# Performance work log

Hardware: AMD Instinct MI355X
Metric: run time of the kernel (lower is better)

Reference implementation:

```python
import jax, jax.numpy as jnp
import numpy as np

T, B, D, H = 1024, 256, 64, 128  # seq_len, batch, x_dim, dim_RNN (= dense dims)


def _linear_params(key, fan_in, fan_out):
    # torch nn.Linear/nn.RNN default init: U(-1/sqrt(fan_in), 1/sqrt(fan_in))
    s = 1.0 / np.sqrt(fan_in)
    kw, kb = jax.random.split(key)
    W = jax.random.uniform(kw, (fan_out, fan_in), minval=-s, maxval=s, dtype=jnp.float32)
    b = jax.random.uniform(kb, (fan_out,), minval=-s, maxval=s, dtype=jnp.float32)
    return W, b


def setup_inputs() -> dict:
    key = jax.random.key(0)
    kx, k1, k2, k3, k4, k5 = jax.random.split(key, 6)
    x = jax.random.normal(kx, (T, B, D), dtype=jnp.float32)
    W_x, b_x = _linear_params(k1, D, H)      # feature_extractor_x: Linear(D->H)
    W_ih, b_ih = _linear_params(k2, H, H)    # RNN input-hidden
    W_hh, b_hh = _linear_params(k3, H, H)    # RNN hidden-hidden
    W_h, b_h = _linear_params(k4, H, H)      # mlp_h_x: Linear(H->H)
    W_g, b_g = _linear_params(k5, H, D)      # gen_out: Linear(H->D)
    return {"x": x, "W_x": W_x, "b_x": b_x, "W_ih": W_ih, "b_ih": b_ih,
            "W_hh": W_hh, "b_hh": b_hh, "W_h": W_h, "b_h": b_h,
            "W_g": W_g, "b_g": b_g}


def reference(x, W_x, b_x, W_ih, b_ih, W_hh, b_hh, W_h, b_h, W_g, b_g):
    # feature extractor applied to all timesteps at once (as in the original)
    feat = jnp.tanh(x @ W_x.T + b_x)                       # [T, B, H]
    batch = x.shape[1]
    h0 = jnp.zeros((batch, W_hh.shape[0]), dtype=x.dtype)  # [B, H]

    def step(h, f_t):
        # y_t is produced from h BEFORE the recurrence update (y[0] uses h=0)
        y_t = jnp.tanh(h @ W_h.T + b_h) @ W_g.T + b_g      # [B, D]
        h_next = jnp.tanh(f_t @ W_ih.T + b_ih + h @ W_hh.T + b_hh)
        return h_next, y_t

    _, y = jax.lax.scan(step, h0, feat)                    # y: [T, B, D]
    return y
```

## Files before the change

### kernel.cpp

```cpp
#include <hip/hip_runtime.h>


#define T_SEQ 1024
#define B_SZ  256
#define D_IN  64
#define H_DIM 128

typedef __attribute__((ext_vector_type(8))) _Float16 half8;
typedef __attribute__((ext_vector_type(4))) _Float16 half4;
typedef __attribute__((ext_vector_type(4))) float f32x4;

__device__ __forceinline__ float fast_tanh(float x) {
  float ax = __builtin_fabsf(x);
  float e  = __builtin_amdgcn_exp2f(ax * -2.8853900817779268f);
  float r  = (1.0f - e) * __builtin_amdgcn_rcpf(1.0f + e);
  return __builtin_copysignf(r, x);
}

__device__ __forceinline__ void barrier_lds_only() {
  __asm__ __volatile__("" ::: "memory");
  __builtin_amdgcn_s_waitcnt(0xC07F);
  __builtin_amdgcn_s_barrier();
  __asm__ __volatile__("" ::: "memory");
}

__device__ __forceinline__ half8 pack_h8(float4 a, float4 b) {
  half8 s = { (_Float16)a.x, (_Float16)a.y, (_Float16)a.z, (_Float16)a.w,
              (_Float16)b.x, (_Float16)b.y, (_Float16)b.z, (_Float16)b.w };
  return s;
}
__device__ __forceinline__ half4 cvt_h4(float4 a) {
  half4 s = { (_Float16)a.x, (_Float16)a.y, (_Float16)a.z, (_Float16)a.w };
  return s;
}
__device__ __forceinline__ void split_h8(float4 a, float4 b, half8& hi, half8& lo) {
  hi = pack_h8(a, b);
  float4 ra = { a.x - (float)hi[0], a.y - (float)hi[1],
                a.z - (float)hi[2], a.w - (float)hi[3] };
  float4 rb = { b.x - (float)hi[4], b.y - (float)hi[5],
                b.z - (float)hi[6], b.w - (float)hi[7] };
  lo = pack_h8(ra, rb);
}

__device__ __forceinline__ float add_xor1(float x) {
  int v = __builtin_amdgcn_mov_dpp(__float_as_int(x), 0xB1, 0xF, 0xF, true);
  return x + __int_as_float(v);
}
__device__ __forceinline__ float add_xor2(float x) {
  int v = __builtin_amdgcn_mov_dpp(__float_as_int(x), 0x4E, 0xF, 0xF, true);
  return x + __int_as_float(v);
}
__device__ __forceinline__ float add_mirror8(float x) {
  int v = __builtin_amdgcn_mov_dpp(__float_as_int(x), 0x141, 0xF, 0xF, true);
  return x + __int_as_float(v);
}
__device__ __forceinline__ float dot4(float4 w, float4 h) {
  return fmaf(w.x, h.x, fmaf(w.y, h.y, fmaf(w.z, h.z, w.w * h.w)));
}

__global__ __launch_bounds__(512) void k_fused(
    const float* __restrict__ x,   const float* __restrict__ Wx,
    const float* __restrict__ bx,  const float* __restrict__ Wih,
    const float* __restrict__ bih, const float* __restrict__ Whh,
    const float* __restrict__ bhh, const float* __restrict__ Wh,
    const float* __restrict__ bh,  const float* __restrict__ Wg,
    const float* __restrict__ bg,  float* __restrict__ y)
{
  __shared__ __align__(16) float    hbuf[2][192];
  __shared__ __align__(16) float    zringT[4][H_DIM][20];
  __shared__ __align__(16) _Float16 hring[4][16][136];
  __shared__ __align__(16) _Float16 xt_h[16][72];
  __shared__ __align__(16) _Float16 xt_l[16][72];
  __shared__ __align__(16) _Float16 fm_h[16][136];
  __shared__ __align__(16) _Float16 fm_l[16][136];
  __shared__ __align__(16) _Float16 tpm[16][136];

  const int tid = threadIdx.x;
  const int b   = blockIdx.x;
  const int wv  = tid >> 6;

  if (wv < 4) {
    const int jg = tid >> 3, ks = tid & 7, k0p = ks * 24;
    const bool writer = (ks < 4);
    const int j_out = jg + (ks & 3) * 32;
    const int j_pad = j_out + ((j_out >> 4) << 3);

    float4 w[4][4];
#pragma unroll
    for (int r = 0; r < 4; ++r) {
      const float4* wg = (const float4*)(Whh + (jg + r*32)*H_DIM + ks*16);
#pragma unroll
      for (int m = 0; m < 4; ++m) w[r][m] = wg[m];
    }
    if (tid < 128) hbuf[0][tid + ((tid >> 4) << 3)] = 0.f;
    else           hring[0][0][tid - 128] = (_Float16)0.f;

    __builtin_amdgcn_s_setprio(1);
    for (int i = 0; i < 5; ++i) barrier_lds_only();

    for (int g = 0; g < 64; ++g) {
      float zbuf[16];
      if (writer) {
        const float* zp = &zringT[g & 3][j_out][0];
        const float4 z0 = *(const float4*)(zp + 0);
        const float4 z1 = *(const float4*)(zp + 4);
        const float4 z2 = *(const float4*)(zp + 8);
        const float4 z3 = *(const float4*)(zp + 12);
        zbuf[0]=z0.x;  zbuf[1]=z0.y;  zbuf[2]=z0.z;  zbuf[3]=z0.w;
        zbuf[4]=z1.x;  zbuf[5]=z1.y;  zbuf[6]=z1.z;  zbuf[7]=z1.w;
        zbuf[8]=z2.x;  zbuf[9]=z2.y;  zbuf[10]=z2.z; zbuf[11]=z2.w;
        zbuf[12]=z3.x; zbuf[13]=z3.y; zbuf[14]=z3.z; zbuf[15]=z3.w;
      }
#pragma unroll
      for (int s = 0; s < 16; ++s) {
        const float* h = hbuf[s & 1];
        float4 h0 = *(const float4*)&h[k0p];
        float4 h1 = *(const float4*)&h[k0p + 4];
        float4 h2 = *(const float4*)&h[k0p + 8];
        float4 h3 = *(const float4*)&h[k0p + 12];

        float a[4];
#pragma unroll
        for (int r = 0; r < 4; ++r) {
          float p0 = dot4(w[r][0], h0);
          float p1 = dot4(w[r][1], h1);
          float p2 = dot4(w[r][2], h2);
          float p3 = dot4(w[r][3], h3);
          a[r] = (p0 + p1) + (p2 + p3);
        }
#pragma unroll
        for (int r = 0; r < 4; ++r) {
          a[r] = add_xor1(a[r]);
          a[r] = add_xor2(a[r]);
          a[r] = add_mirror8(a[r]);
        }
        if (writer) {
          float v  = a[ks] + zbuf[s];
          float hn = fast_tanh(v);
          hbuf[(s & 1) ^ 1][j_pad] = hn;
          const int tn = g*16 + s + 1;
          hring[(tn >> 4) & 3][tn & 15][j_out] = (_Float16)hn;
        }
        barrier_lds_only();
      }
    }
    barrier_lds_only();

  } else if (wv < 6) {
    const int l = tid & 63, ln = l & 15, kg = l >> 4;
    const int pw = wv - 4;
    const int xr0 = pw*8 + kg;

    half8 wxh[4][2], wxl[4][2];
    float bxr[4], b2r[4];
#pragma unroll
    for (int nt = 0; nt < 4; ++nt) {
      const int ro = (pw*4 + nt)*16 + ln;
#pragma unroll
      for (int kf = 0; kf < 2; ++kf) {
        const float* wp = Wx + ro*D_IN + kf*32 + kg*8;
        split_h8(*(const float4*)wp, *(const float4*)(wp + 4),
                 wxh[nt][kf], wxl[nt][kf]);
      }
      bxr[nt] = bx[ro];
      b2r[nt] = bih[ro] + bhh[ro];
    }

    float4 xa0, xa1;
    float4 lw[16];

    auto loadx = [&](int t0) {
      xa0 = *(const float4*)(x + ((long)(t0 + xr0    )*B_SZ + b)*D_IN + ln*4);
      xa1 = *(const float4*)(x + ((long)(t0 + xr0 + 4)*B_SZ + b)*D_IN + ln*4);
    };
    auto cvtx = [&]() {
      half4 h0 = cvt_h4(xa0);
      float4 r0 = { xa0.x - (float)h0[0], xa0.y - (float)h0[1],
                    xa0.z - (float)h0[2], xa0.w - (float)h0[3] };
      *(half4*)&xt_h[xr0][ln*4] = h0;
      *(half4*)&xt_l[xr0][ln*4] = cvt_h4(r0);
      half4 h1 = cvt_h4(xa1);
      float4 r1 = { xa1.x - (float)h1[0], xa1.y - (float)h1[1],
                    xa1.z - (float)h1[2], xa1.w - (float)h1[3] };
      *(half4*)&xt_h[xr0 + 4][ln*4] = h1;
      *(half4*)&xt_l[xr0 + 4][ln*4] = cvt_h4(r1);
    };
    auto st1 = [&]() {
      half8 a1h[2], a1l[2];
#pragma unroll
      for (int kf = 0; kf < 2; ++kf) {
        a1h[kf] = *(const half8*)&xt_h[ln][kf*32 + kg*8];
        a1l[kf] = *(const half8*)&xt_l[ln][kf*32 + kg*8];
      }
#pragma unroll
      for (int nt = 0; nt < 4; ++nt) {
        f32x4 acc = {0.f, 0.f, 0.f, 0.f};
#pragma unroll
        for (int kf = 0; kf < 2; ++kf) {
          acc = __builtin_amdgcn_mfma_f32_16x16x32_f16(a1h[kf], wxh[nt][kf], acc, 0, 0, 0);
          acc = __builtin_amdgcn_mfma_f32_16x16x32_f16(a1l[kf], wxh[nt][kf], acc, 0, 0, 0);
          acc = __builtin_amdgcn_mfma_f32_16x16x32_f16(a1h[kf], wxl[nt][kf], acc, 0, 0, 0);
        }
#pragma unroll
        for (int c = 0; c < 4; ++c) {
          float v = fast_tanh(acc[c] + bxr[nt]);
          _Float16 vh = (_Float16)v;
          fm_h[kg*4 + c][(pw*4 + nt)*16 + ln] = vh;
          fm_l[kg*4 + c][(pw*4 + nt)*16 + ln] = (_Float16)(v - (float)vh);
        }
      }
    };
    auto ld2 = [&](int nt0) {
#pragma unroll
      for (int i = 0; i < 2; ++i) {
        const int ro = (pw*4 + nt0 + i)*16 + ln;
#pragma unroll
        for (int kf = 0; kf < 4; ++kf) {
          const float* wp = Wih + ro*H_DIM + kf*32 + kg*8;
          lw[i*8 + kf*2 + 0] = *(const float4*)wp;
          lw[i*8 + kf*2 + 1] = *(const float4*)(wp + 4);
        }
      }
    };
    auto use2 = [&](int nt0, int slot) {
      half8 a2h[4], a2l[4];
#pragma unroll
      for (int kf = 0; kf < 4; ++kf) {
        a2h[kf] = *(const half8*)&fm_h[ln][kf*32 + kg*8];
        a2l[kf] = *(const half8*)&fm_l[ln][kf*32 + kg*8];
      }
#pragma unroll
      for (int i = 0; i < 2; ++i) {
        const int nt = nt0 + i;
        const int ro = (pw*4 + nt)*16 + ln;
        f32x4 acc = { b2r[nt], b2r[nt], b2r[nt], b2r[nt] };
#pragma unroll
        for (int kf = 0; kf < 4; ++kf) {
          half8 bh_, bl_;
          split_h8(lw[i*8 + kf*2], lw[i*8 + kf*2 + 1], bh_, bl_);
          acc = __builtin_amdgcn_mfma_f32_16x16x32_f16(a2h[kf], bh_, acc, 0, 0, 0);
          acc = __builtin_amdgcn_mfma_f32_16x16x32_f16(a2l[kf], bh_, acc, 0, 0, 0);
          acc = __builtin_amdgcn_mfma_f32_16x16x32_f16(a2h[kf], bl_, acc, 0, 0, 0);
        }
        *(f32x4*)&zringT[slot][ro][kg*4] = acc;
      }
    };

    loadx(0);
    cvtx(); loadx(16);            barrier_lds_only();
    st1();                        barrier_lds_only();
    ld2(0); use2(0, 0); ld2(2); use2(2, 0);
    cvtx(); loadx(32);            barrier_lds_only();
    st1();                        barrier_lds_only();
    ld2(0); use2(0, 1); ld2(2); use2(2, 1);
                                  barrier_lds_only();

    for (int g = 0; g < 64; ++g) {
      const bool act = (g <= 61);
      const int slot = (g + 2) & 3;
      if (act) cvtx();
      if (g <= 60) loadx((g + 3) * 16);
      barrier_lds_only();
      if (act) { ld2(0); st1(); }
      barrier_lds_only();
      if (act) { use2(0, slot); ld2(2); }
      barrier_lds_only();
      if (act) use2(2, slot);
      barrier_lds_only();
      for (int s = 4; s < 16; ++s) barrier_lds_only();
    }
    barrier_lds_only();

  } else {
    const int l = tid & 63, ln = l & 15, kg = l >> 4;
    const int cw = wv - 6;

    float bhr[4], bgr[2];
#pragma unroll
    for (int nt = 0; nt < 4; ++nt) bhr[nt] = bh[(cw*4 + nt)*16 + ln];
#pragma unroll
    for (int n2 = 0; n2 < 2; ++n2) bgr[n2] = bg[(cw*2 + n2)*16 + ln];

    float4 lwc[16];

    auto ldc1 = [&](int nt0) {
#pragma unroll
      for (int i = 0; i < 2; ++i) {
        const int ro = (cw*4 + nt0 + i)*16 + ln;
#pragma unroll
        for (int kf = 0; kf < 4; ++kf) {
          const float* wp = Wh + ro*H_DIM + kf*32 + kg*8;
          lwc[i*8 + kf*2 + 0] = *(const float4*)wp;
          lwc[i*8 + kf*2 + 1] = *(const float4*)(wp + 4);
        }
      }
    };
    auto usec1 = [&](int nt0, int slot) {
      half8 ah[4];
#pragma unroll
      for (int kf = 0; kf < 4; ++kf)
        ah[kf] = *(const half8*)&hring[slot][ln][kf*32 + kg*8];
#pragma unroll
      for (int i = 0; i < 2; ++i) {
        const int nt = nt0 + i;
        f32x4 acc = {0.f, 0.f, 0.f, 0.f};
#pragma unroll
        for (int kf = 0; kf < 4; ++kf) {
          half8 bh_, bl_;
          split_h8(lwc[i*8 + kf*2], lwc[i*8 + kf*2 + 1], bh_, bl_);
          acc = __builtin_amdgcn_mfma_f32_16x16x32_f16(ah[kf], bh_, acc, 0, 0, 0);
          acc = __builtin_amdgcn_mfma_f32_16x16x32_f16(ah[kf], bl_, acc, 0, 0, 0);
        }
#pragma unroll
        for (int c = 0; c < 4; ++c)
          tpm[kg*4 + c][(cw*4 + nt)*16 + ln] =
              (_Float16)fast_tanh(acc[c] + bhr[nt]);
      }
    };
    auto ldc2 = [&]() {
#pragma unroll
      for (int i = 0; i < 2; ++i) {
        const int ro = (cw*2 + i)*16 + ln;
#pragma unroll
        for (int kf = 0; kf < 4; ++kf) {
          const float* wp = Wg + ro*H_DIM + kf*32 + kg*8;
          lwc[i*8 + kf*2 + 0] = *(const float4*)wp;
          lwc[i*8 + kf*2 + 1] = *(const float4*)(wp + 4);
        }
      }
    };
    auto usec2 = [&](int t0) {
      half8 atp[4];
#pragma unroll
      for (int kf = 0; kf < 4; ++kf)
        atp[kf] = *(const half8*)&tpm[ln][kf*32 + kg*8];
#pragma unroll
      for (int n2 = 0; n2 < 2; ++n2) {
        f32x4 acc = { bgr[n2], bgr[n2], bgr[n2], bgr[n2] };
#pragma unroll
        for (int kf = 0; kf < 4; ++kf) {
          half8 bh_, bl_;
          split_h8(lwc[n2*8 + kf*2], lwc[n2*8 + kf*2 + 1], bh_, bl_);
          acc = __builtin_amdgcn_mfma_f32_16x16x32_f16(atp[kf], bh_, acc, 0, 0, 0);
          acc = __builtin_amdgcn_mfma_f32_16x16x32_f16(atp[kf], bl_, acc, 0, 0, 0);
        }
#pragma unroll
        for (int c = 0; c < 4; ++c)
          y[((long)(t0 + kg*4 + c)*B_SZ + b)*D_IN + (cw*2 + n2)*16 + ln] = acc[c];
      }
    };

    for (int i = 0; i < 5; ++i) barrier_lds_only();

    for (int g = 0; g < 64; ++g) {
      const bool act = (g >= 1);
      const int slot = (g - 1) & 3;
      const int t0 = (g - 1) * 16;
      barrier_lds_only();
      barrier_lds_only();
      barrier_lds_only();
      barrier_lds_only();
      barrier_lds_only();
      barrier_lds_only();
      if (act) ldc1(0);
      barrier_lds_only();
      if (act) { usec1(0, slot); ldc1(2); }
      barrier_lds_only();
      if (act) { usec1(2, slot); ldc2(); }
      barrier_lds_only();
      barrier_lds_only();
      if (act) usec2(t0);
      barrier_lds_only();
      for (int s = 11; s < 16; ++s) barrier_lds_only();
    }
    ldc1(0); usec1(0, 3); ldc1(2); usec1(2, 3);
    barrier_lds_only();
    ldc2(); usec2(63 * 16);
  }
}

extern "C" void kernel_launch(void* const* d_in, const int* in_sizes, int n_in,
                              void* d_out, int out_size, void* d_ws, size_t ws_size,
                              hipStream_t stream) {
  const float* x   = (const float*)d_in[0];
  const float* Wx  = (const float*)d_in[1];
  const float* bx  = (const float*)d_in[2];
  const float* Wih = (const float*)d_in[3];
  const float* bih = (const float*)d_in[4];
  const float* Whh = (const float*)d_in[5];
  const float* bhh = (const float*)d_in[6];
  const float* Wh  = (const float*)d_in[7];
  const float* bh  = (const float*)d_in[8];
  const float* Wg  = (const float*)d_in[9];
  const float* bg  = (const float*)d_in[10];
  float* y = (float*)d_out;

  k_fused<<<B_SZ, 512, 0, stream>>>(x, Wx, bx, Wih, bih, Whh, bhh,
                                    Wh, bh, Wg, bg, y);
}
```

Baseline: 655.5 us.

## Split producer and consumer warp work into finer per-tile stages across barriers

```diff
diff --git a/kernel.cpp b/kernel.cpp
--- a/kernel.cpp
+++ b/kernel.cpp
@@ -167,7 +167,8 @@
     }
 
     float4 xa0, xa1;
-    float4 lw[16];
+    half8 a1h[2], a1l[2], a2h[4], a2l[4];
+    float4 lwA[8], lwB[8];
 
     auto loadx = [&](int t0) {
       xa0 = *(const float4*)(x + ((long)(t0 + xr0    )*B_SZ + b)*D_IN + ln*4);
@@ -185,15 +186,16 @@
       *(half4*)&xt_h[xr0 + 4][ln*4] = h1;
       *(half4*)&xt_l[xr0 + 4][ln*4] = cvt_h4(r1);
     };
-    auto st1 = [&]() {
-      half8 a1h[2], a1l[2];
+    auto rd_a1 = [&]() {
 #pragma unroll
       for (int kf = 0; kf < 2; ++kf) {
         a1h[kf] = *(const half8*)&xt_h[ln][kf*32 + kg*8];
         a1l[kf] = *(const half8*)&xt_l[ln][kf*32 + kg*8];
       }
-#pragma unroll
-      for (int nt = 0; nt < 4; ++nt) {
+    };
+    auto st1_h = [&](int nt0) {
+#pragma unroll
+      for (int nt = nt0; nt < nt0 + 2; ++nt) {
         f32x4 acc = {0.f, 0.f, 0.f, 0.f};
 #pragma unroll
         for (int kf = 0; kf < 2; ++kf) {
@@ -210,64 +212,72 @@
         }
       }
     };
-    auto ld2 = [&](int nt0) {
-#pragma unroll
-      for (int i = 0; i < 2; ++i) {
-        const int ro = (pw*4 + nt0 + i)*16 + ln;
-#pragma unroll
-        for (int kf = 0; kf < 4; ++kf) {
-          const float* wp = Wih + ro*H_DIM + kf*32 + kg*8;
-          lw[i*8 + kf*2 + 0] = *(const float4*)wp;
-          lw[i*8 + kf*2 + 1] = *(const float4*)(wp + 4);
-        }
-      }
-    };
-    auto use2 = [&](int nt0, int slot) {
-      half8 a2h[4], a2l[4];
+    auto rd_a2 = [&]() {
 #pragma unroll
       for (int kf = 0; kf < 4; ++kf) {
         a2h[kf] = *(const half8*)&fm_h[ln][kf*32 + kg*8];
         a2l[kf] = *(const half8*)&fm_l[ln][kf*32 + kg*8];
       }
-#pragma unroll
-      for (int i = 0; i < 2; ++i) {
-        const int nt = nt0 + i;
-        const int ro = (pw*4 + nt)*16 + ln;
-        f32x4 acc = { b2r[nt], b2r[nt], b2r[nt], b2r[nt] };
-#pragma unroll
-        for (int kf = 0; kf < 4; ++kf) {
-          half8 bh_, bl_;
-          split_h8(lw[i*8 + kf*2], lw[i*8 + kf*2 + 1], bh_, bl_);
-          acc = __builtin_amdgcn_mfma_f32_16x16x32_f16(a2h[kf], bh_, acc, 0, 0, 0);
-          acc = __builtin_amdgcn_mfma_f32_16x16x32_f16(a2l[kf], bh_, acc, 0, 0, 0);
-          acc = __builtin_amdgcn_mfma_f32_16x16x32_f16(a2h[kf], bl_, acc, 0, 0, 0);
-        }
-        *(f32x4*)&zringT[slot][ro][kg*4] = acc;
-      }
+    };
+    auto ldq = [&](float4* lw, int nt) {
+      const int ro = (pw*4 + nt)*16 + ln;
+      const float* wp0 = Wih + ro*H_DIM;
+#pragma unroll
+      for (int kf = 0; kf < 4; ++kf) {
+        lw[kf*2 + 0] = *(const float4*)(wp0 + kf*32 + kg*8);
+        lw[kf*2 + 1] = *(const float4*)(wp0 + kf*32 + kg*8 + 4);
+      }
+    };
+    auto use2_q = [&](const float4* lw, int nt, int slot) {
+      const int ro = (pw*4 + nt)*16 + ln;
+      f32x4 acc = { b2r[nt], b2r[nt], b2r[nt], b2r[nt] };
+#pragma unroll
+      for (int kf = 0; kf < 4; ++kf) {
+        half8 bh_, bl_;
+        split_h8(lw[kf*2], lw[kf*2 + 1], bh_, bl_);
+        acc = __builtin_amdgcn_mfma_f32_16x16x32_f16(a2h[kf], bh_, acc, 0, 0, 0);
+        acc = __builtin_amdgcn_mfma_f32_16x16x32_f16(a2l[kf], bh_, acc, 0, 0, 0);
+        acc = __builtin_amdgcn_mfma_f32_16x16x32_f16(a2h[kf], bl_, acc, 0, 0, 0);
+      }
+      *(f32x4*)&zringT[slot][ro][kg*4] = acc;
     };
 
     loadx(0);
-    cvtx(); loadx(16);            barrier_lds_only();
-    st1();                        barrier_lds_only();
-    ld2(0); use2(0, 0); ld2(2); use2(2, 0);
-    cvtx(); loadx(32);            barrier_lds_only();
-    st1();                        barrier_lds_only();
-    ld2(0); use2(0, 1); ld2(2); use2(2, 1);
-                                  barrier_lds_only();
+    cvtx(); loadx(16);                       barrier_lds_only();
+    rd_a1(); st1_h(0); st1_h(2);             barrier_lds_only();
+    rd_a2();
+    ldq(lwA, 0); use2_q(lwA, 0, 0);
+    ldq(lwA, 1); use2_q(lwA, 1, 0);
+    ldq(lwA, 2); use2_q(lwA, 2, 0);
+    ldq(lwA, 3); use2_q(lwA, 3, 0);
+    cvtx(); loadx(32);                       barrier_lds_only();
+    rd_a1(); st1_h(0); st1_h(2);             barrier_lds_only();
+    rd_a2();
+    ldq(lwA, 0); use2_q(lwA, 0, 1);
+    ldq(lwA, 1); use2_q(lwA, 1, 1);
+    ldq(lwA, 2); use2_q(lwA, 2, 1);
+    ldq(lwA, 3); use2_q(lwA, 3, 1);
+                                             barrier_lds_only();
 
     for (int g = 0; g < 64; ++g) {
       const bool act = (g <= 61);
       const int slot = (g + 2) & 3;
-      if (act) cvtx();
+      if (act) { cvtx(); ldq(lwA, 0); }
       if (g <= 60) loadx((g + 3) * 16);
       barrier_lds_only();
-      if (act) { ld2(0); st1(); }
-      barrier_lds_only();
-      if (act) { use2(0, slot); ld2(2); }
-      barrier_lds_only();
-      if (act) use2(2, slot);
-      barrier_lds_only();
-      for (int s = 4; s < 16; ++s) barrier_lds_only();
+      if (act) { rd_a1(); st1_h(0); ldq(lwB, 1); }
+      barrier_lds_only();
+      if (act) st1_h(2);
+      barrier_lds_only();
+      if (act) { rd_a2(); use2_q(lwA, 0, slot); ldq(lwA, 2); }
+      barrier_lds_only();
+      if (act) { use2_q(lwB, 1, slot); ldq(lwB, 3); }
+      barrier_lds_only();
+      if (act) use2_q(lwA, 2, slot);
+      barrier_lds_only();
+      if (act) use2_q(lwB, 3, slot);
+      barrier_lds_only();
+      for (int s = 7; s < 16; ++s) barrier_lds_only();
     }
     barrier_lds_only();
 
@@ -281,73 +291,65 @@
 #pragma unroll
     for (int n2 = 0; n2 < 2; ++n2) bgr[n2] = bg[(cw*2 + n2)*16 + ln];
 
-    float4 lwc[16];
-
-    auto ldc1 = [&](int nt0) {
-#pragma unroll
-      for (int i = 0; i < 2; ++i) {
-        const int ro = (cw*4 + nt0 + i)*16 + ln;
-#pragma unroll
-        for (int kf = 0; kf < 4; ++kf) {
-          const float* wp = Wh + ro*H_DIM + kf*32 + kg*8;
-          lwc[i*8 + kf*2 + 0] = *(const float4*)wp;
-          lwc[i*8 + kf*2 + 1] = *(const float4*)(wp + 4);
-        }
-      }
-    };
-    auto usec1 = [&](int nt0, int slot) {
-      half8 ah[4];
+    half8 ah[4], atp[4];
+    float4 lcA[8], lcB[8];
+
+    auto rd_ah = [&](int slot) {
 #pragma unroll
       for (int kf = 0; kf < 4; ++kf)
         ah[kf] = *(const half8*)&hring[slot][ln][kf*32 + kg*8];
-#pragma unroll
-      for (int i = 0; i < 2; ++i) {
-        const int nt = nt0 + i;
-        f32x4 acc = {0.f, 0.f, 0.f, 0.f};
-#pragma unroll
-        for (int kf = 0; kf < 4; ++kf) {
-          half8 bh_, bl_;
-          split_h8(lwc[i*8 + kf*2], lwc[i*8 + kf*2 + 1], bh_, bl_);
-          acc = __builtin_amdgcn_mfma_f32_16x16x32_f16(ah[kf], bh_, acc, 0, 0, 0);
-          acc = __builtin_amdgcn_mfma_f32_16x16x32_f16(ah[kf], bl_, acc, 0, 0, 0);
-        }
-#pragma unroll
-        for (int c = 0; c < 4; ++c)
-          tpm[kg*4 + c][(cw*4 + nt)*16 + ln] =
-              (_Float16)fast_tanh(acc[c] + bhr[nt]);
-      }
-    };
-    auto ldc2 = [&]() {
-#pragma unroll
-      for (int i = 0; i < 2; ++i) {
-        const int ro = (cw*2 + i)*16 + ln;
-#pragma unroll
-        for (int kf = 0; kf < 4; ++kf) {
-          const float* wp = Wg + ro*H_DIM + kf*32 + kg*8;
-          lwc[i*8 + kf*2 + 0] = *(const float4*)wp;
-          lwc[i*8 + kf*2 + 1] = *(const float4*)(wp + 4);
-        }
-      }
-    };
-    auto usec2 = [&](int t0) {
-      half8 atp[4];
+    };
+    auto ldc = [&](float4* lc, int nt) {
+      const int ro = (cw*4 + nt)*16 + ln;
+      const float* wp0 = Wh + ro*H_DIM;
+#pragma unroll
+      for (int kf = 0; kf < 4; ++kf) {
+        lc[kf*2 + 0] = *(const float4*)(wp0 + kf*32 + kg*8);
+        lc[kf*2 + 1] = *(const float4*)(wp0 + kf*32 + kg*8 + 4);
+      }
+    };
+    auto usec1_q = [&](const float4* lc, int nt) {
+      f32x4 acc = {0.f, 0.f, 0.f, 0.f};
+#pragma unroll
+      for (int kf = 0; kf < 4; ++kf) {
+        half8 bh_, bl_;
+        split_h8(lc[kf*2], lc[kf*2 + 1], bh_, bl_);
+        acc = __builtin_amdgcn_mfma_f32_16x16x32_f16(ah[kf], bh_, acc, 0, 0, 0);
+        acc = __builtin_amdgcn_mfma_f32_16x16x32_f16(ah[kf], bl_, acc, 0, 0, 0);
+      }
+#pragma unroll
+      for (int c = 0; c < 4; ++c)
+        tpm[kg*4 + c][(cw*4 + nt)*16 + ln] =
+            (_Float16)fast_tanh(acc[c] + bhr[nt]);
+    };
+    auto ldcg = [&]() {
+#pragma unroll
+      for (int kf = 0; kf < 4; ++kf) {
+        const float* wp0 = Wg + ((cw*2 + 0)*16 + ln)*H_DIM + kf*32 + kg*8;
+        lcA[kf*2 + 0] = *(const float4*)wp0;
+        lcA[kf*2 + 1] = *(const float4*)(wp0 + 4);
+        const float* wp1 = Wg + ((cw*2 + 1)*16 + ln)*H_DIM + kf*32 + kg*8;
+        lcB[kf*2 + 0] = *(const float4*)wp1;
+        lcB[kf*2 + 1] = *(const float4*)(wp1 + 4);
+      }
+    };
+    auto rd_atp = [&]() {
 #pragma unroll
       for (int kf = 0; kf < 4; ++kf)
         atp[kf] = *(const half8*)&tpm[ln][kf*32 + kg*8];
-#pragma unroll
-      for (int n2 = 0; n2 < 2; ++n2) {
-        f32x4 acc = { bgr[n2], bgr[n2], bgr[n2], bgr[n2] };
-#pragma unroll
-        for (int kf = 0; kf < 4; ++kf) {
-          half8 bh_, bl_;
-          split_h8(lwc[n2*8 + kf*2], lwc[n2*8 + kf*2 + 1], bh_, bl_);
-          acc = __builtin_amdgcn_mfma_f32_16x16x32_f16(atp[kf], bh_, acc, 0, 0, 0);
-          acc = __builtin_amdgcn_mfma_f32_16x16x32_f16(atp[kf], bl_, acc, 0, 0, 0);
-        }
-#pragma unroll
-        for (int c = 0; c < 4; ++c)
-          y[((long)(t0 + kg*4 + c)*B_SZ + b)*D_IN + (cw*2 + n2)*16 + ln] = acc[c];
-      }
+    };
+    auto usec2_h = [&](const float4* lc, int n2, int t0) {
+      f32x4 acc = { bgr[n2], bgr[n2], bgr[n2], bgr[n2] };
+#pragma unroll
+      for (int kf = 0; kf < 4; ++kf) {
+        half8 bh_, bl_;
+        split_h8(lc[kf*2], lc[kf*2 + 1], bh_, bl_);
+        acc = __builtin_amdgcn_mfma_f32_16x16x32_f16(atp[kf], bh_, acc, 0, 0, 0);
+        acc = __builtin_amdgcn_mfma_f32_16x16x32_f16(atp[kf], bl_, acc, 0, 0, 0);
+      }
+#pragma unroll
+      for (int c = 0; c < 4; ++c)
+        y[((long)(t0 + kg*4 + c)*B_SZ + b)*D_IN + (cw*2 + n2)*16 + ln] = acc[c];
     };
 
     for (int i = 0; i < 5; ++i) barrier_lds_only();
@@ -362,20 +364,32 @@
       barrier_lds_only();
       barrier_lds_only();
       barrier_lds_only();
-      if (act) ldc1(0);
-      barrier_lds_only();
-      if (act) { usec1(0, slot); ldc1(2); }
-      barrier_lds_only();
-      if (act) { usec1(2, slot); ldc2(); }
-      barrier_lds_only();
-      barrier_lds_only();
-      if (act) usec2(t0);
-      barrier_lds_only();
-      for (int s = 11; s < 16; ++s) barrier_lds_only();
+      if (act) { rd_ah(slot); ldc(lcA, 0); }
+      barrier_lds_only();
+      if (act) { usec1_q(lcA, 0); ldc(lcB, 1); }
+      barrier_lds_only();
+      if (act) { usec1_q(lcB, 1); ldc(lcA, 2); }
+      barrier_lds_only();
+      if (act) { usec1_q(lcA, 2); ldc(lcB, 3); }
+      barrier_lds_only();
+      if (act) { usec1_q(lcB, 3); ldcg(); }
+      barrier_lds_only();
+      if (act) { rd_atp(); usec2_h(lcA, 0, t0); }
+      barrier_lds_only();
+      if (act) usec2_h(lcB, 1, t0);
+      barrier_lds_only();
+      barrier_lds_only();
+      barrier_lds_only();
+      barrier_lds_only();
     }
-    ldc1(0); usec1(0, 3); ldc1(2); usec1(2, 3);
+    rd_ah(3);
+    ldc(lcA, 0); usec1_q(lcA, 0);
+    ldc(lcB, 1); usec1_q(lcB, 1);
+    ldc(lcA, 2); usec1_q(lcA, 2);
+    ldc(lcB, 3); usec1_q(lcB, 3);
+    ldcg();
     barrier_lds_only();
-    ldc2(); usec2(63 * 16);
+    rd_atp(); usec2_h(lcA, 0, 63 * 16); usec2_h(lcB, 1, 63 * 16);
   }
 }
 
```

New measurement: 662.5 us. No clear change (+1.1%).
